# Performance work log

Measured on AMD Instinct MI355X. Metric: run time of the kernel, lower is better.

The kernel has to match this reference:

```python
import math
import jax, jax.numpy as jnp
import numpy as np

B, H, W, C = 16, 64, 64, 256


def setup_inputs() -> dict:
    key = jax.random.key(0)
    ks = jax.random.split(key, 6)
    return {
        "h": jax.random.normal(ks[0], (B, H, W, C), jnp.float32),
        # grouped 3x3 perception conv: groups=C, in/groups=1, out=3C
        "w_perc": jax.random.normal(ks[1], (3 * C, 1, 3, 3), jnp.float32) * 0.1,
        "b_perc": jnp.zeros((3 * C,), jnp.float32),
        # update_net: 1x1 conv 3C->2C, GELU, 1x1 conv 2C->C
        "w_up1": jax.random.normal(ks[2], (2 * C, 3 * C, 1, 1), jnp.float32) * 0.02,
        "b_up1": jnp.zeros((2 * C,), jnp.float32),
        "w_up2": jax.random.normal(ks[3], (C, 2 * C, 1, 1), jnp.float32) * 0.02,
        "b_up2": jnp.zeros((C,), jnp.float32),
        # lin_qkv: Linear C -> 3C (torch weight layout [out,in])
        "w_qkv": jax.random.normal(ks[4], (3 * C, C), jnp.float32) * 0.02,
        "b_qkv": jnp.zeros((3 * C,), jnp.float32),
    }


_POS = [(-1, -1), (-1, 0), (-1, 1), (0, -1), (0, 0), (0, 1), (1, -1), (1, 0), (1, 1)]


def _local_attn(hn, w_qkv, b_qkv):
    """3x3 windowed local attention (zero-padded borders), NHWC in/out."""
    Bb, Hh, Ww, Cc = hn.shape
    qkv = jnp.einsum('bhwc,dc->bhwd', hn, w_qkv) + b_qkv
    q, k, v = jnp.split(qkv, 3, axis=-1)
    kp = jnp.pad(k, ((0, 0), (1, 1), (1, 1), (0, 0)))
    vp = jnp.pad(v, ((0, 0), (1, 1), (1, 1), (0, 0)))
    scale = 1.0 / math.sqrt(Cc)
    # scores over the 9 neighbor offsets -> [B,H,W,9]
    scores = jnp.stack(
        [(q * kp[:, 1 + dy:1 + dy + Hh, 1 + dx:1 + dx + Ww, :]).sum(-1) for dy, dx in _POS],
        axis=-1) * scale
    w = jax.nn.softmax(scores, axis=-1)
    out = jnp.zeros_like(v)
    for i, (dy, dx) in enumerate(_POS):
        out = out + w[..., i:i + 1] * vp[:, 1 + dy:1 + dy + Hh, 1 + dx:1 + dx + Ww, :]
    return out


def reference(h, w_perc, b_perc, w_up1, b_up1, w_up2, b_up2, w_qkv, b_qkv):
    # eval-mode forward: noise / dropout / stochastic mask are identity
    Cc = h.shape[-1]
    x = jnp.transpose(h, (0, 3, 1, 2))  # NCHW
    perceived = jax.lax.conv_general_dilated(
        x, w_perc, window_strides=(1, 1), padding='SAME',
        feature_group_count=Cc,
        dimension_numbers=('NCHW', 'OIHW', 'NCHW')) + b_perc[None, :, None, None]
    hid = jnp.einsum('bphw,dp->bdhw', perceived, w_up1[:, :, 0, 0]) + b_up1[None, :, None, None]
    hid = jax.nn.gelu(hid, approximate=False)
    dx = jnp.einsum('bdhw,cd->bchw', hid, w_up2[:, :, 0, 0]) + b_up2[None, :, None, None]
    x_new = x + dx  # stochastic_update in eval mode
    h_new = jnp.transpose(x_new, (0, 2, 3, 1))  # NHWC
    h_attn = _local_attn(h_new, w_qkv, b_qkv)
    return h_new + h_attn
```

## Files before the change

### kernel.cpp

```cpp
#include <hip/hip_runtime.h>
#include <math.h>


typedef unsigned short u16;
typedef __bf16 bf16x8 __attribute__((ext_vector_type(8)));
typedef float floatx4 __attribute__((ext_vector_type(4)));

__device__ int g_flag;
__device__ __align__(16) u16 g_h[16777216];
__device__ __align__(16) u16 g_perc[50331648];
__device__ __align__(16) u16 g_hid[33554432];
__device__ __align__(16) u16 g_hnew[16777216];
__device__ __align__(16) u16 g_wperc[6912];
__device__ __align__(16) u16 g_bperc[768];
__device__ __align__(16) u16 g_wup1[393216];
__device__ __align__(16) u16 g_bup1[512];
__device__ __align__(16) u16 g_wup2[131072];
__device__ __align__(16) u16 g_bup2[256];
__device__ __align__(16) u16 g_wqkv[196608];
__device__ __align__(16) u16 g_bqkv[768];

__device__ __forceinline__ float b2f(u16 x) {
  unsigned int u = ((unsigned int)x) << 16;
  float f;
  __builtin_memcpy(&f, &u, 4);
  return f;
}
__device__ __forceinline__ u16 f2b(float f) {
  unsigned int u;
  __builtin_memcpy(&u, &f, 4);
  u += 0x7FFFu + ((u >> 16) & 1u);
  return (u16)(u >> 16);
}
__device__ __forceinline__ void gload16(const u16* g, u16* l) {
  __builtin_amdgcn_global_load_lds(
      (const __attribute__((address_space(1))) unsigned int*)g,
      (__attribute__((address_space(3))) unsigned int*)l, 16, 0, 0);
}
__device__ __forceinline__ void ld8(const u16* p, float* f) {
  uint4 v = *(const uint4*)p;
  f[0] = b2f((u16)(v.x & 0xFFFF)); f[1] = b2f((u16)(v.x >> 16));
  f[2] = b2f((u16)(v.y & 0xFFFF)); f[3] = b2f((u16)(v.y >> 16));
  f[4] = b2f((u16)(v.z & 0xFFFF)); f[5] = b2f((u16)(v.z >> 16));
  f[6] = b2f((u16)(v.w & 0xFFFF)); f[7] = b2f((u16)(v.w >> 16));
}

__global__ __launch_bounds__(256) void probe_kernel(const u16* __restrict__ h) {
  __shared__ int hit;
  if (threadIdx.x == 0) hit = 0;
  __syncthreads();
  int local = 0;
  for (int i = threadIdx.x; i < 8192; i += 256) {
    u16 v = h[2 * i];
    if ((v & 0x7F80) == 0x7F80) local = 1;
  }
  if (local) atomicOr(&hit, 1);
  __syncthreads();
  if (threadIdx.x == 0) g_flag = hit;
}

__global__ __launch_bounds__(256) void conv_w_kernel(
    const void* i1, const void* i2, const void* i3, const void* i4,
    const void* i5, const void* i6, const void* i7, const void* i8) {
  const void* srcs[8] = {i1, i2, i3, i4, i5, i6, i7, i8};
  u16* dsts[8] = {g_wperc, g_bperc, g_wup1, g_bup1,
                  g_wup2,  g_bup2,  g_wqkv, g_bqkv};
  const int szs[8] = {6912, 768, 393216, 512, 131072, 256, 196608, 768};
  const int fp32 = g_flag;
  const int stride = gridDim.x * 256;
  for (int gw = blockIdx.x * 256 + threadIdx.x; gw < 730112; gw += stride) {
    int seg = 0, off = gw;
    while (off >= szs[seg]) { off -= szs[seg]; ++seg; }
    dsts[seg][off] = fp32 ? f2b(((const float*)srcs[seg])[off])
                          : ((const u16*)srcs[seg])[off];
  }
}

__global__ __launch_bounds__(256) void perc_kernel(const void* __restrict__ hin) {
  __shared__ __align__(16) u16 sw[3456];
  __shared__ __align__(16) u16 sb[384];
  const int bid = blockIdx.x >> 1;
  const int chalf = blockIdx.x & 1;
  const int b = bid >> 6, y = bid & 63;
  const int xi = threadIdx.x >> 6;
  const int cl = threadIdx.x & 63;
  const int c0 = chalf * 128 + cl * 2;
  for (int i = threadIdx.x; i < 3456; i += 256) sw[i] = g_wperc[chalf * 3456 + i];
  for (int i = threadIdx.x; i < 384; i += 256) sb[i] = g_bperc[chalf * 384 + i];
  const int fp32 = g_flag;
  __syncthreads();
  float w[2][27], bias[2][3];
#pragma unroll
  for (int ch = 0; ch < 2; ++ch) {
    const int lc = cl * 2 + ch;
#pragma unroll
    for (int t = 0; t < 3; ++t) {
      bias[ch][t] = b2f(sb[3 * lc + t]);
#pragma unroll
      for (int j = 0; j < 9; ++j)
        w[ch][t * 9 + j] = b2f(sw[(3 * lc + t) * 9 + j]);
    }
  }
  float hv[3][3][2];
  auto loadcol = [&](int xx, int cc) {
#pragma unroll
    for (int r = 0; r < 3; ++r) {
      const int yy = y - 1 + r;
      const bool ok = ((unsigned)yy < 64u) && ((unsigned)xx < 64u);
      if (ok) {
        const size_t idx = (((size_t)(b * 64 + yy) * 64) + xx) * 256 + c0;
        if (fp32) {
          const float2 v = *(const float2*)((const float*)hin + idx);
          hv[r][cc][0] = v.x;
          hv[r][cc][1] = v.y;
        } else {
          const unsigned v = *(const unsigned*)((const u16*)hin + idx);
          hv[r][cc][0] = b2f((u16)(v & 0xFFFF));
          hv[r][cc][1] = b2f((u16)(v >> 16));
        }
      } else {
        hv[r][cc][0] = 0.0f;
        hv[r][cc][1] = 0.0f;
      }
    }
  };
  const int x0 = xi * 16;
  loadcol(x0 - 1, 0);
  loadcol(x0, 1);
#pragma unroll
  for (int k = 0; k < 16; ++k) {
    const int x = x0 + k;
    loadcol(x + 1, (k + 2) % 3);
    const int cL = k % 3, cM = (k + 1) % 3, cR = (k + 2) % 3;
    const size_t pix = (size_t)(b * 64 + y) * 64 + x;
    *(unsigned*)&g_h[pix * 256 + c0] =
        (unsigned)f2b(hv[1][cM][0]) | ((unsigned)f2b(hv[1][cM][1]) << 16);
    u16* op = &g_perc[pix * 768 + 3 * c0];
    unsigned pk[3];
#pragma unroll
    for (int ch = 0; ch < 2; ++ch) {
#pragma unroll
      for (int t = 0; t < 3; ++t) {
        const float* wt = &w[ch][t * 9];
        float a = bias[ch][t];
        a += hv[0][cL][ch] * wt[0] + hv[0][cM][ch] * wt[1] + hv[0][cR][ch] * wt[2];
        a += hv[1][cL][ch] * wt[3] + hv[1][cM][ch] * wt[4] + hv[1][cR][ch] * wt[5];
        a += hv[2][cL][ch] * wt[6] + hv[2][cM][ch] * wt[7] + hv[2][cR][ch] * wt[8];
        const int o = 3 * ch + t;
        const unsigned bb = f2b(a);
        if (o & 1) pk[o >> 1] |= bb << 16; else pk[o >> 1] = bb;
      }
    }
    *(unsigned*)(op) = pk[0];
    *(unsigned*)(op + 2) = pk[1];
    *(unsigned*)(op + 4) = pk[2];
  }
}

template <int MODE, int NB>
__global__ __launch_bounds__(256) void gemm_bt(int K) {
  const u16 *A, *Bw, *bias, *resid;
  u16* C;
  if (MODE == 0) { A = g_perc; Bw = g_wup1; bias = g_bup1; resid = nullptr; C = g_hid; }
  if (MODE == 1) { A = g_hid;  Bw = g_wup2; bias = g_bup2; resid = g_h;     C = g_hnew; }
  if (MODE == 2) { A = g_hnew; Bw = g_wqkv; bias = g_bqkv; resid = nullptr; C = g_perc; }
  const int N = NB * 128;

  __shared__ __align__(16) u16 Al[128 * 64];
  __shared__ __align__(16) u16 Bl[128 * 64];
  const int tid = threadIdx.x;
  const int wave = tid >> 6, lane = tid & 63;
  const int ln = lane & 15, quad = lane >> 4;
  const int lnx = ln & 7;
  const int mb_per_xcd = (gridDim.x / NB) >> 3;
  const int m_blk = (blockIdx.x & 7) * mb_per_xcd + (blockIdx.x >> 3) / NB;
  const int n_blk = (blockIdx.x >> 3) % NB;
  const int m0 = m_blk * 128, n0 = n_blk * 128;
  const int wm = (wave >> 1) * 64, wn = (wave & 1) * 64;
  floatx4 acc[4][4] = {};

  int srow[4], scol[4];
#pragma unroll
  for (int r = 0; r < 4; ++r) {
    const int slot = r * 256 + tid;
    srow[r] = slot >> 3;
    scol[r] = ((slot & 7) ^ (srow[r] & 7)) * 8;
  }

  for (int k0 = 0; k0 < K; k0 += 64) {
#pragma unroll
    for (int r = 0; r < 4; ++r)
      gload16(&A[(size_t)(m0 + srow[r]) * K + k0 + scol[r]],
              &Al[(r * 256 + tid) * 8]);
#pragma unroll
    for (int r = 0; r < 4; ++r)
      gload16(&Bw[(size_t)(n0 + srow[r]) * K + k0 + scol[r]],
              &Bl[(r * 256 + tid) * 8]);
    __syncthreads();
#pragma unroll
    for (int kk8 = 0; kk8 < 8; kk8 += 4) {
      bf16x8 af[4], bfr[4];
#pragma unroll
      for (int i = 0; i < 4; ++i) {
        const int row = wm + i * 16 + ln;
        af[i] = *(const bf16x8*)(&Al[(row * 8 + ((kk8 + quad) ^ lnx)) * 8]);
      }
#pragma unroll
      for (int j = 0; j < 4; ++j) {
        const int row = wn + j * 16 + ln;
        bfr[j] = *(const bf16x8*)(&Bl[(row * 8 + ((kk8 + quad) ^ lnx)) * 8]);
      }
#pragma unroll
      for (int i = 0; i < 4; ++i)
#pragma unroll
        for (int j = 0; j < 4; ++j)
          acc[i][j] = __builtin_amdgcn_mfma_f32_16x16x32_bf16(af[i], bfr[j],
                                                              acc[i][j], 0, 0, 0);
    }
    __syncthreads();
  }

#pragma unroll
  for (int i = 0; i < 4; ++i) {
#pragma unroll
    for (int rr = 0; rr < 4; ++rr) {
      const int m = m0 + wm + i * 16 + quad * 4 + rr;
#pragma unroll
      for (int j = 0; j < 4; ++j) {
        const int n = n0 + wn + j * 16 + ln;
        float v = acc[i][j][rr] + b2f(bias[n]);
        if (MODE == 0) v = 0.5f * v * (1.0f + erff(v * 0.70710678118654752f));
        if (MODE == 1) v += b2f(resid[(size_t)m * N + n]);
        C[(size_t)m * N + n] = f2b(v);
      }
    }
  }
}

__global__ __launch_bounds__(256) void attn_kernel(void* __restrict__ outv) {
  const int wv = threadIdx.x >> 6, lane = threadIdx.x & 63;
  const int half = lane >> 5, cl = lane & 31;
  const int c0 = cl * 8;
  const int pix = blockIdx.x * 8 + wv * 2 + half;
  const int y = (pix >> 6) & 63, x = pix & 63;
  float q[8];
  ld8(g_perc + (size_t)pix * 768 + c0, q);
  float s[9];
  int nidx[9];
#pragma unroll
  for (int j = 0; j < 9; ++j) {
    const int dy = j / 3 - 1, dx = j % 3 - 1;
    const int yy = y + dy, xx = x + dx;
    const bool ok = ((unsigned)yy < 64u) && ((unsigned)xx < 64u);
    const int np = pix + dy * 64 + dx;
    nidx[j] = ok ? np : -1;
    float p = 0.0f;
    if (ok) {
      float kv[8];
      ld8(g_perc + (size_t)np * 768 + 256 + c0, kv);
      p = q[0] * kv[0] + q[1] * kv[1] + q[2] * kv[2] + q[3] * kv[3] +
          q[4] * kv[4] + q[5] * kv[5] + q[6] * kv[6] + q[7] * kv[7];
    }
#pragma unroll
    for (int off = 16; off >= 1; off >>= 1) p += __shfl_xor(p, off, 64);
    s[j] = p * 0.0625f;
  }
  float mx = s[0];
#pragma unroll
  for (int j = 1; j < 9; ++j) mx = fmaxf(mx, s[j]);
  float e[9], den = 0.0f;
#pragma unroll
  for (int j = 0; j < 9; ++j) {
    e[j] = expf(s[j] - mx);
    den += e[j];
  }
  const float inv = 1.0f / den;
  float a[8];
  ld8(g_hnew + (size_t)pix * 256 + c0, a);
#pragma unroll
  for (int j = 0; j < 9; ++j) {
    if (nidx[j] >= 0) {
      const float wgt = e[j] * inv;
      float vv[8];
      ld8(g_perc + (size_t)nidx[j] * 768 + 512 + c0, vv);
#pragma unroll
      for (int t = 0; t < 8; ++t) a[t] += wgt * vv[t];
    }
  }
  const size_t o = (size_t)pix * 256 + c0;
  if (g_flag) {
    float4 r0 = {a[0], a[1], a[2], a[3]};
    float4 r1 = {a[4], a[5], a[6], a[7]};
    *(float4*)((float*)outv + o) = r0;
    *(float4*)((float*)outv + o + 4) = r1;
  } else {
    uint4 r;
    r.x = (unsigned)f2b(a[0]) | ((unsigned)f2b(a[1]) << 16);
    r.y = (unsigned)f2b(a[2]) | ((unsigned)f2b(a[3]) << 16);
    r.z = (unsigned)f2b(a[4]) | ((unsigned)f2b(a[5]) << 16);
    r.w = (unsigned)f2b(a[6]) | ((unsigned)f2b(a[7]) << 16);
    *(uint4*)((u16*)outv + o) = r;
  }
}

extern "C" void kernel_launch(void* const* d_in, const int* in_sizes, int n_in,
                              void* d_out, int d_out_size, void* d_ws,
                              size_t ws_size, hipStream_t stream) {
  (void)d_ws; (void)ws_size;
  probe_kernel<<<1, 256, 0, stream>>>((const u16*)d_in[0]);
  conv_w_kernel<<<360, 256, 0, stream>>>(d_in[1], d_in[2], d_in[3], d_in[4],
                                         d_in[5], d_in[6], d_in[7], d_in[8]);
  perc_kernel<<<2048, 256, 0, stream>>>(d_in[0]);
  gemm_bt<0, 4><<<2048, 256, 0, stream>>>(768);
  gemm_bt<1, 2><<<1024, 256, 0, stream>>>(512);
  gemm_bt<2, 6><<<3072, 256, 0, stream>>>(256);
  attn_kernel<<<8192, 256, 0, stream>>>(d_out);
}
```

Before: 429.5 us.

## Rewrite GEMMs as 256x256 tiles with 8 waves and double-buffered async LDS pipeline

Replaces the 128x128 single-buffered GEMM with a 256x256 tile computed by 512 threads (8 waves). K-tiles are double-buffered in LDS and loaded asynchronously in quarter-tile stages that interleave with MFMA sub-blocks, using manual vmcnt waits and barriers plus setprio around the MFMA bursts. The larger tile cuts global traffic per FLOP, and the pipeline hides load latency. The cost is 64KB of LDS and more accumulator registers, which lowers occupancy. Grid sizes shrink to match, so the launch count is small relative to CU count, which risks tail imbalance.

```diff
diff --git a/kernel.cpp b/kernel.cpp
--- a/kernel.cpp
+++ b/kernel.cpp
@@ -158,80 +158,120 @@
 }
 
 template <int MODE, int NB>
-__global__ __launch_bounds__(256) void gemm_bt(int K) {
+__global__ __launch_bounds__(512) void gemm_bt(int K) {
   const u16 *A, *Bw, *bias, *resid;
   u16* C;
   if (MODE == 0) { A = g_perc; Bw = g_wup1; bias = g_bup1; resid = nullptr; C = g_hid; }
   if (MODE == 1) { A = g_hid;  Bw = g_wup2; bias = g_bup2; resid = g_h;     C = g_hnew; }
   if (MODE == 2) { A = g_hnew; Bw = g_wqkv; bias = g_bqkv; resid = nullptr; C = g_perc; }
-  const int N = NB * 128;
-
-  __shared__ __align__(16) u16 Al[128 * 64];
-  __shared__ __align__(16) u16 Bl[128 * 64];
+  const int N = NB * 256;
+  const int NT = K >> 6;
+
+  __shared__ __align__(16) u16 lds[2][2][2][8192];
   const int tid = threadIdx.x;
-  const int wave = tid >> 6, lane = tid & 63;
-  const int ln = lane & 15, quad = lane >> 4;
-  const int lnx = ln & 7;
+  const int w = tid >> 6, lane = tid & 63;
+  const int ln = lane & 15, quad = lane >> 4, lnx = ln & 7;
+  const int wmi = w >> 2, wni = w & 3;
+
   const int mb_per_xcd = (gridDim.x / NB) >> 3;
   const int m_blk = (blockIdx.x & 7) * mb_per_xcd + (blockIdx.x >> 3) / NB;
   const int n_blk = (blockIdx.x >> 3) % NB;
-  const int m0 = m_blk * 128, n0 = n_blk * 128;
-  const int wm = (wave >> 1) * 64, wn = (wave & 1) * 64;
-  floatx4 acc[4][4] = {};
-
-  int srow[4], scol[4];
-#pragma unroll
-  for (int r = 0; r < 4; ++r) {
-    const int slot = r * 256 + tid;
-    srow[r] = slot >> 3;
-    scol[r] = ((slot & 7) ^ (srow[r] & 7)) * 8;
-  }
-
-  for (int k0 = 0; k0 < K; k0 += 64) {
-#pragma unroll
-    for (int r = 0; r < 4; ++r)
-      gload16(&A[(size_t)(m0 + srow[r]) * K + k0 + scol[r]],
-              &Al[(r * 256 + tid) * 8]);
-#pragma unroll
-    for (int r = 0; r < 4; ++r)
-      gload16(&Bw[(size_t)(n0 + srow[r]) * K + k0 + scol[r]],
-              &Bl[(r * 256 + tid) * 8]);
-    __syncthreads();
-#pragma unroll
-    for (int kk8 = 0; kk8 < 8; kk8 += 4) {
-      bf16x8 af[4], bfr[4];
-#pragma unroll
-      for (int i = 0; i < 4; ++i) {
-        const int row = wm + i * 16 + ln;
-        af[i] = *(const bf16x8*)(&Al[(row * 8 + ((kk8 + quad) ^ lnx)) * 8]);
-      }
-#pragma unroll
-      for (int j = 0; j < 4; ++j) {
-        const int row = wn + j * 16 + ln;
-        bfr[j] = *(const bf16x8*)(&Bl[(row * 8 + ((kk8 + quad) ^ lnx)) * 8]);
-      }
-#pragma unroll
-      for (int i = 0; i < 4; ++i)
-#pragma unroll
-        for (int j = 0; j < 4; ++j)
-          acc[i][j] = __builtin_amdgcn_mfma_f32_16x16x32_bf16(af[i], bfr[j],
-                                                              acc[i][j], 0, 0, 0);
-    }
-    __syncthreads();
-  }
-
-#pragma unroll
-  for (int i = 0; i < 4; ++i) {
-#pragma unroll
-    for (int rr = 0; rr < 4; ++rr) {
-      const int m = m0 + wm + i * 16 + quad * 4 + rr;
-#pragma unroll
-      for (int j = 0; j < 4; ++j) {
-        const int n = n0 + wn + j * 16 + ln;
-        float v = acc[i][j][rr] + b2f(bias[n]);
+  const int m0 = m_blk * 256, n0 = n_blk * 256;
+
+  auto stageA = [&](int t, int half) {
+    u16* dst = &lds[t & 1][0][half][0];
+#pragma unroll
+    for (int ld = 0; ld < 2; ++ld) {
+      const int s = ld * 512 + tid;
+      const int srow = s >> 3, sch = (s & 7) ^ (srow & 7);
+      gload16(&A[(size_t)(m0 + half * 128 + srow) * K + t * 64 + sch * 8],
+              dst + s * 8);
+    }
+  };
+  auto stageB = [&](int t, int half) {
+    u16* dst = &lds[t & 1][1][half][0];
+#pragma unroll
+    for (int ld = 0; ld < 2; ++ld) {
+      const int s = ld * 512 + tid;
+      const int srow = s >> 3, sch = (s & 7) ^ (srow & 7);
+      gload16(&Bw[(size_t)(n0 + half * 128 + srow) * K + t * 64 + sch * 8],
+              dst + s * 8);
+    }
+  };
+
+  floatx4 acc[8][4] = {};
+  bf16x8 af[4][2], bfr[2][2];
+
+  stageA(0, 0); stageB(0, 1); stageA(0, 1); stageB(0, 0);
+  stageA(1, 0); stageB(1, 1);
+
+  for (int u = 0; u < NT; ++u) {
+    const u16* Abuf = &lds[u & 1][0][0][0];
+    const u16* Bbuf = &lds[u & 1][1][0][0];
+#pragma unroll
+    for (int r = 0; r < 4; ++r) {
+      if (r == 0 && u + 1 < NT) stageA(u + 1, 1);
+      if (r == 1 && u + 1 < NT) stageB(u + 1, 0);
+      if (r == 2 && u + 2 < NT) stageA(u + 2, 0);
+      if (r == 3 && u + 2 < NT) stageB(u + 2, 1);
+      if (r == 0) {
+        if (u + 1 < NT) asm volatile("s_waitcnt vmcnt(6)" ::: "memory");
+        else            asm volatile("s_waitcnt vmcnt(0)" ::: "memory");
+      }
+      asm volatile("s_barrier" ::: "memory");
+      const int ah = (r >= 2) ? 1 : 0;
+      const int bh = (r == 1 || r == 2) ? 1 : 0;
+      if (r == 0 || r == 2) {
+#pragma unroll
+        for (int f2 = 0; f2 < 4; ++f2) {
+          const int row = (f2 * 2 + wmi) * 16 + ln;
+#pragma unroll
+          for (int ks = 0; ks < 2; ++ks) {
+            const int ch = (ks * 4 + quad) ^ lnx;
+            af[f2][ks] = *(const bf16x8*)(Abuf + ah * 8192 + (row * 8 + ch) * 8);
+          }
+        }
+      }
+      if (r != 2) {
+#pragma unroll
+        for (int g2 = 0; g2 < 2; ++g2) {
+          const int row = (g2 * 4 + wni) * 16 + ln;
+#pragma unroll
+          for (int ks = 0; ks < 2; ++ks) {
+            const int ch = (ks * 4 + quad) ^ lnx;
+            bfr[g2][ks] = *(const bf16x8*)(Bbuf + bh * 8192 + (row * 8 + ch) * 8);
+          }
+        }
+      }
+      __builtin_amdgcn_s_setprio(1);
+#pragma unroll
+      for (int f2 = 0; f2 < 4; ++f2)
+#pragma unroll
+        for (int g2 = 0; g2 < 2; ++g2)
+#pragma unroll
+          for (int ks = 0; ks < 2; ++ks)
+            acc[ah * 4 + f2][bh * 2 + g2] =
+                __builtin_amdgcn_mfma_f32_16x16x32_bf16(
+                    af[f2][ks], bfr[g2][ks], acc[ah * 4 + f2][bh * 2 + g2],
+                    0, 0, 0);
+      __builtin_amdgcn_s_setprio(0);
+      asm volatile("s_barrier" ::: "memory");
+    }
+  }
+
+#pragma unroll
+  for (int f = 0; f < 8; ++f) {
+    const int mB = m0 + (f * 2 + wmi) * 16 + quad * 4;
+#pragma unroll
+    for (int g = 0; g < 4; ++g) {
+      const int n = n0 + (g * 4 + wni) * 16 + ln;
+      const float bv = b2f(bias[n]);
+#pragma unroll
+      for (int rr = 0; rr < 4; ++rr) {
+        float v = acc[f][g][rr] + bv;
         if (MODE == 0) v = 0.5f * v * (1.0f + erff(v * 0.70710678118654752f));
-        if (MODE == 1) v += b2f(resid[(size_t)m * N + n]);
-        C[(size_t)m * N + n] = f2b(v);
+        if (MODE == 1) v += b2f(resid[(size_t)(mB + rr) * N + n]);
+        C[(size_t)(mB + rr) * N + n] = f2b(v);
       }
     }
   }
@@ -311,8 +351,8 @@
   conv_w_kernel<<<360, 256, 0, stream>>>(d_in[1], d_in[2], d_in[3], d_in[4],
                                          d_in[5], d_in[6], d_in[7], d_in[8]);
   perc_kernel<<<2048, 256, 0, stream>>>(d_in[0]);
-  gemm_bt<0, 4><<<2048, 256, 0, stream>>>(768);
-  gemm_bt<1, 2><<<1024, 256, 0, stream>>>(512);
-  gemm_bt<2, 6><<<3072, 256, 0, stream>>>(256);
+  gemm_bt<0, 2><<<512, 512, 0, stream>>>(768);
+  gemm_bt<1, 1><<<256, 512, 0, stream>>>(512);
+  gemm_bt<2, 3><<<768, 512, 0, stream>>>(256);
   attn_kernel<<<8192, 256, 0, stream>>>(d_out);
 }
```

Result: no change. 422.2 us (-1.7%).
